# Optimization experiments

Hardware: AMD Instinct MI355X
Metric: run time of the kernel (lower is better)

## Reference

```python
import jax, jax.numpy as jnp
import numpy as np

B, S, H, NH = 4, 2048, 1024, 16
HD = H // NH

def setup_inputs() -> dict:
    key = jax.random.key(0)
    ks = jax.random.split(key, 9)
    s = 1.0 / np.sqrt(H)
    return {
        "x": jax.random.normal(ks[0], (B, S, H), dtype=jnp.float32),
        "Wq": jax.random.uniform(ks[1], (H, H), jnp.float32, -s, s),
        "bq": jax.random.uniform(ks[2], (H,), jnp.float32, -s, s),
        "Wk": jax.random.uniform(ks[3], (H, H), jnp.float32, -s, s),
        "bk": jax.random.uniform(ks[4], (H,), jnp.float32, -s, s),
        "Wv": jax.random.uniform(ks[5], (H, H), jnp.float32, -s, s),
        "bv": jax.random.uniform(ks[6], (H,), jnp.float32, -s, s),
        "Wo": jax.random.uniform(ks[7], (H, H), jnp.float32, -s, s),
        "bo": jax.random.uniform(ks[8], (H,), jnp.float32, -s, s),
    }

def reference(x, Wq, bq, Wk, bk, Wv, bv, Wo, bo):
    b, s, h = x.shape
    scale = np.sqrt(HD).astype(np.float32)
    def split_heads(t):  # [b,s,h] -> [b,nh,s,hd]
        return t.reshape(b, s, NH, HD).transpose(0, 2, 1, 3)
    Q = split_heads(x @ Wq.T + bq)
    K = split_heads(x @ Wk.T + bk)
    V = split_heads(x @ Wv.T + bv)
    scores = jnp.einsum('bnqd,bnkd->bnqk', Q, K) / scale
    weights = jax.nn.softmax(scores, axis=-1)
    attn = jnp.einsum('bnqk,bnkd->bnqd', weights, V)
    attn = attn.transpose(0, 2, 1, 3).reshape(b, s, h)
    return attn @ Wo.T + bo
```

## Files before the change

### kernel.cpp

```cpp
#include <hip/hip_runtime.h>
#include <cstdint>

#define BB 4
#define SS 2048
#define HH 1024
#define NHH 16
#define HDD 64

typedef __bf16 bf16x8 __attribute__((ext_vector_type(8)));
typedef float f32x4 __attribute__((ext_vector_type(4)));
typedef unsigned short u16x8 __attribute__((ext_vector_type(8)));

__device__ __forceinline__ unsigned short f2b(float f) {
    unsigned int u = __float_as_uint(f);
    u += 0x7fffu + ((u >> 16) & 1u);
    return (unsigned short)(u >> 16);
}

__device__ __forceinline__ void gload_lds16(const void* g, void* l) {
    __builtin_amdgcn_global_load_lds(
        (const __attribute__((address_space(1))) void*)g,
        (__attribute__((address_space(3))) void*)l, 16, 0, 0);
}

__global__ void cvt_bf16(const float* __restrict__ in,
                         unsigned short* __restrict__ out, long n) {
    long i = ((long)blockIdx.x * blockDim.x + threadIdx.x) * 4;
    long stride = (long)gridDim.x * blockDim.x * 4;
    for (; i < n; i += stride) {
        float4 v = *reinterpret_cast<const float4*>(in + i);
        ushort4 o;
        o.x = f2b(v.x); o.y = f2b(v.y); o.z = f2b(v.z); o.w = f2b(v.w);
        *reinterpret_cast<ushort4*>(out + i) = o;
    }
}

__global__ void cvt_w4(const float* __restrict__ w0, const float* __restrict__ w1,
                       const float* __restrict__ w2, const float* __restrict__ w3,
                       unsigned short* __restrict__ out) {
    const float* s = blockIdx.y == 0 ? w0 : blockIdx.y == 1 ? w1 : blockIdx.y == 2 ? w2 : w3;
    unsigned short* o = out + (size_t)blockIdx.y * ((size_t)HH * HH);
    long n = (long)HH * HH;
    long stride = (long)gridDim.x * blockDim.x * 4;
    for (long i = ((long)blockIdx.x * blockDim.x + threadIdx.x) * 4; i < n; i += stride) {
        float4 v = *reinterpret_cast<const float4*>(s + i);
        ushort4 w;
        w.x = f2b(v.x); w.y = f2b(v.y); w.z = f2b(v.z); w.w = f2b(v.w);
        *reinterpret_cast<ushort4*>(o + i) = w;
    }
}

__global__ __launch_bounds__(256) void gemm_qkv(
    const unsigned short* __restrict__ A,
    const unsigned short* __restrict__ Bqkv,
    const float* __restrict__ bq, const float* __restrict__ bk,
    const float* __restrict__ bv,
    unsigned short* __restrict__ Qo, unsigned short* __restrict__ Ko,
    unsigned short* __restrict__ Vto)
{
    __shared__ alignas(16) unsigned short Al[2][128][32];
    __shared__ alignas(16) unsigned short Bl[2][128][32];

    const int tid = threadIdx.x;
    const int lane = tid & 63;
    const int wid  = tid >> 6;
    const int wm = wid >> 1, wn = wid & 1;
    const int l15 = lane & 15, g = lane >> 4;

    const int wg = blockIdx.x;
    const int x = wg & 7;
    const int local = wg >> 3;
    const int row0 = ((x & 3) * 16 + local / 12) * 128;
    const int col0 = ((x >> 2) * 12 + local % 12) * 128;
    const int nb = col0 >> 10;
    const int cbase = col0 & 1023;
    const float* bias = nb == 0 ? bq : nb == 1 ? bk : bv;
    const int K = HH;

    f32x4 acc[4][4];
#pragma unroll
    for (int i = 0; i < 4; i++)
#pragma unroll
        for (int j = 0; j < 4; j++) acc[i][j] = (f32x4)0.0f;

    const int off0 = tid * 16;
    const int aoff0 = (off0 >> 6) * (K * 2) + (off0 & 63);
    const int off1 = off0 + 4096;
    const int aoff1 = (off1 >> 6) * (K * 2) + (off1 & 63);

    const char* gAb = (const char*)(A + (size_t)row0 * K);
    const char* gBb = (const char*)(Bqkv + (size_t)col0 * K);

    auto STAGE = [&](int buf, int k0) {
        const char* a = gAb + k0 * 64;
        const char* bsrc = gBb + k0 * 64;
        char* lA = (char*)&Al[buf][0][0] + wid * 1024;
        char* lB = (char*)&Bl[buf][0][0] + wid * 1024;
        gload_lds16(a + aoff0, lA);
        gload_lds16(a + aoff1, lA + 4096);
        gload_lds16(bsrc + aoff0, lB);
        gload_lds16(bsrc + aoff1, lB + 4096);
    };

    STAGE(0, 0);
    __syncthreads();
    int cur = 0;

    for (int k = 0; k < 32; k++) {
        if (k + 1 < 32) STAGE(cur ^ 1, k + 1);

        bf16x8 af[4], bf[4];
#pragma unroll
        for (int i = 0; i < 4; i++)
            af[i] = *reinterpret_cast<const bf16x8*>(&Al[cur][wm * 64 + i * 16 + l15][g * 8]);
#pragma unroll
        for (int j = 0; j < 4; j++)
            bf[j] = *reinterpret_cast<const bf16x8*>(&Bl[cur][wn * 64 + j * 16 + l15][g * 8]);
#pragma unroll
        for (int i = 0; i < 4; i++)
#pragma unroll
            for (int j = 0; j < 4; j++)
                acc[i][j] = __builtin_amdgcn_mfma_f32_16x16x32_bf16(af[i], bf[j], acc[i][j], 0, 0, 0);
        __syncthreads();
        cur ^= 1;
    }

#pragma unroll
    for (int i = 0; i < 4; i++) {
#pragma unroll
        for (int j = 0; j < 4; j++) {
#pragma unroll
            for (int r = 0; r < 4; r++) {
                int row = row0 + wm * 64 + i * 16 + g * 4 + r;
                int col = cbase + wn * 64 + j * 16 + l15;
                float v = acc[i][j][r] + bias[col];
                if (nb == 0) {
                    Qo[(size_t)row * HH + col] = f2b(v);
                } else if (nb == 1) {
                    Ko[(size_t)row * HH + col] = f2b(v);
                } else {
                    int b = row >> 11;
                    int s = row & (SS - 1);
                    int s6 = s & 63;
                    int sp6 = (s6 & 0x23) | ((s6 & 0x0C) << 1) | ((s6 & 0x10) >> 2);
                    int head = col >> 6;
                    int d = col & (HDD - 1);
                    size_t idx = (((size_t)b * NHH + head) * HDD + d) * SS + (s & ~63) + sp6;
                    Vto[idx] = f2b(v);
                }
            }
        }
    }
}

__global__ __launch_bounds__(256) void gemm_out(
    const unsigned short* __restrict__ A,
    const unsigned short* __restrict__ Bm,
    const float* __restrict__ bias,
    float* __restrict__ Cout,
    int M, int N, int K)
{
    __shared__ alignas(16) unsigned short Al[2][128][32];
    __shared__ alignas(16) unsigned short Bl[2][128][32];

    const int tid = threadIdx.x;
    const int lane = tid & 63;
    const int wid  = tid >> 6;
    const int wm = wid >> 1, wn = wid & 1;
    const int l15 = lane & 15, g = lane >> 4;

    const int wg = blockIdx.x;
    const int x = wg & 7;
    const int local = wg >> 3;
    const int row0 = (x * 8 + local / 8) * 128;
    const int col0 = (local % 8) * 128;

    f32x4 acc[4][4];
#pragma unroll
    for (int i = 0; i < 4; i++)
#pragma unroll
        for (int j = 0; j < 4; j++) acc[i][j] = (f32x4)0.0f;

    const int off0 = tid * 16;
    const int aoff0 = (off0 >> 6) * (K * 2) + (off0 & 63);
    const int off1 = off0 + 4096;
    const int aoff1 = (off1 >> 6) * (K * 2) + (off1 & 63);

    const char* gAb = (const char*)(A + (size_t)row0 * K);
    const char* gBb = (const char*)(Bm + (size_t)col0 * K);

    auto STAGE = [&](int buf, int k0) {
        const char* a = gAb + k0 * 64;
        const char* bsrc = gBb + k0 * 64;
        char* lA = (char*)&Al[buf][0][0] + wid * 1024;
        char* lB = (char*)&Bl[buf][0][0] + wid * 1024;
        gload_lds16(a + aoff0, lA);
        gload_lds16(a + aoff1, lA + 4096);
        gload_lds16(bsrc + aoff0, lB);
        gload_lds16(bsrc + aoff1, lB + 4096);
    };

    STAGE(0, 0);
    __syncthreads();
    int cur = 0;

    for (int k = 0; k < 32; k++) {
        if (k + 1 < 32) STAGE(cur ^ 1, k + 1);

        bf16x8 af[4], bf[4];
#pragma unroll
        for (int i = 0; i < 4; i++)
            af[i] = *reinterpret_cast<const bf16x8*>(&Al[cur][wm * 64 + i * 16 + l15][g * 8]);
#pragma unroll
        for (int j = 0; j < 4; j++)
            bf[j] = *reinterpret_cast<const bf16x8*>(&Bl[cur][wn * 64 + j * 16 + l15][g * 8]);
#pragma unroll
        for (int i = 0; i < 4; i++)
#pragma unroll
            for (int j = 0; j < 4; j++)
                acc[i][j] = __builtin_amdgcn_mfma_f32_16x16x32_bf16(af[i], bf[j], acc[i][j], 0, 0, 0);
        __syncthreads();
        cur ^= 1;
    }

#pragma unroll
    for (int i = 0; i < 4; i++) {
#pragma unroll
        for (int j = 0; j < 4; j++) {
#pragma unroll
            for (int r = 0; r < 4; r++) {
                int row = row0 + wm * 64 + i * 16 + g * 4 + r;
                int col = col0 + wn * 64 + j * 16 + l15;
                Cout[(size_t)row * N + col] = acc[i][j][r] + bias[col];
            }
        }
    }
}

__global__ __launch_bounds__(256, 4) void attn_kernel(
    const unsigned short* __restrict__ Q,
    const unsigned short* __restrict__ K,
    const unsigned short* __restrict__ Vt,
    unsigned short* __restrict__ Oa)
{
    __shared__ alignas(16) unsigned short Kf[2][8][64][8];
    __shared__ alignas(16) unsigned short Vf[2][8][64][8];

    const int tid = threadIdx.x;
    const int lane = tid & 63;
    const int wid  = tid >> 6;
    const int l15 = lane & 15, g = lane >> 4;

    const int wg = blockIdx.x;
    const int L = (wg & 7) * 128 + (wg >> 3);
    const int qt = L & 15;
    const int bh = L >> 4;
    const int b  = bh >> 4;
    const int h  = bh & 15;
    const int q0 = qt * 128;
    const int qA = q0 + wid * 32;

    const float qs = 0.125f * 1.44269504088896f;
    const unsigned short* qpA = Q + (size_t)(b * SS + qA + l15) * HH + h * HDD + g * 8;
    const unsigned short* qpB = qpA + (size_t)16 * HH;
    u16x8 ra0 = *reinterpret_cast<const u16x8*>(qpA);
    u16x8 ra1 = *reinterpret_cast<const u16x8*>(qpA + 32);
    u16x8 rb0 = *reinterpret_cast<const u16x8*>(qpB);
    u16x8 rb1 = *reinterpret_cast<const u16x8*>(qpB + 32);
#pragma unroll
    for (int j = 0; j < 8; j++) {
        ra0[j] = f2b(__uint_as_float((unsigned)ra0[j] << 16) * qs);
        ra1[j] = f2b(__uint_as_float((unsigned)ra1[j] << 16) * qs);
        rb0[j] = f2b(__uint_as_float((unsigned)rb0[j] << 16) * qs);
        rb1[j] = f2b(__uint_as_float((unsigned)rb1[j] << 16) * qs);
    }
    const bf16x8 qa0 = __builtin_bit_cast(bf16x8, ra0);
    const bf16x8 qa1 = __builtin_bit_cast(bf16x8, ra1);
    const bf16x8 qb0 = __builtin_bit_cast(bf16x8, rb0);
    const bf16x8 qb1 = __builtin_bit_cast(bf16x8, rb1);

    u16x8 ou;
#pragma unroll
    for (int j = 0; j < 8; j++) ou[j] = 0x3F80;
    const bf16x8 ones8 = __builtin_bit_cast(bf16x8, ou);
    const f32x4 zero4 = (f32x4)0.0f;

    f32x4 acc_a[4], acc_b[4];
#pragma unroll
    for (int dn = 0; dn < 4; dn++) { acc_a[dn] = zero4; acc_b[dn] = zero4; }
    float m_a = -INFINITY, m_b = -INFINITY, l_a = 0.f, l_b = 0.f;

    const int srow = tid >> 2;
    const int d0a  = (tid & 3) * 2;
    const int sfrag = ((srow >> 4) << 1) + (d0a >> 2);
    const int sslot = (srow & 15) | ((d0a & 3) << 4);

    const unsigned short* gK = K  + (size_t)(b * SS + srow) * HH + h * HDD + d0a * 8;
    const unsigned short* gV = Vt + (((size_t)b * NHH + h) * HDD + srow) * SS + d0a * 8;

    int4 kr0, kr1, vr0, vr1;

    auto stage_write = [&](int buf) {
        unsigned short* pk = &Kf[buf][sfrag][0][0] + sslot * 8;
        unsigned short* pv = &Vf[buf][sfrag][0][0] + sslot * 8;
        *reinterpret_cast<int4*>(pk)       = kr0;
        *reinterpret_cast<int4*>(pk + 128) = kr1;
        *reinterpret_cast<int4*>(pv)       = vr0;
        *reinterpret_cast<int4*>(pv + 128) = vr1;
    };

    kr0 = *reinterpret_cast<const int4*>(gK);
    kr1 = *reinterpret_cast<const int4*>(gK + 8);
    vr0 = *reinterpret_cast<const int4*>(gV);
    vr1 = *reinterpret_cast<const int4*>(gV + 8);
    stage_write(0);
    gK += (size_t)64 * HH;
    gV += 64;
    __syncthreads();

    const int NT = SS / 64;
    int cur = 0;

    for (int kt = 0; kt < NT; kt++) {
        if (kt + 1 < NT) {
            kr0 = *reinterpret_cast<const int4*>(gK);
            kr1 = *reinterpret_cast<const int4*>(gK + 8);
            vr0 = *reinterpret_cast<const int4*>(gV);
            vr1 = *reinterpret_cast<const int4*>(gV + 8);
            gK += (size_t)64 * HH;
            gV += 64;
        }

        f32x4 sa[4], sb[4];
        __builtin_amdgcn_s_setprio(1);
#pragma unroll
        for (int n = 0; n < 4; n++) {
            bf16x8 kf0 = *reinterpret_cast<const bf16x8*>(&Kf[cur][n * 2 + 0][lane][0]);
            bf16x8 kf1 = *reinterpret_cast<const bf16x8*>(&Kf[cur][n * 2 + 1][lane][0]);
            sa[n] = __builtin_amdgcn_mfma_f32_16x16x32_bf16(kf0, qa0, zero4, 0, 0, 0);
            sa[n] = __builtin_amdgcn_mfma_f32_16x16x32_bf16(kf1, qa1, sa[n], 0, 0, 0);
            sb[n] = __builtin_amdgcn_mfma_f32_16x16x32_bf16(kf0, qb0, zero4, 0, 0, 0);
            sb[n] = __builtin_amdgcn_mfma_f32_16x16x32_bf16(kf1, qb1, sb[n], 0, 0, 0);
        }
        __builtin_amdgcn_s_setprio(0);

        bf16x8 pa0, pa1, pb0, pb1;
        {
            float u0 = fmaxf(fmaxf(sa[0][0], sa[0][1]), fmaxf(sa[0][2], sa[0][3]));
            float u1 = fmaxf(fmaxf(sa[1][0], sa[1][1]), fmaxf(sa[1][2], sa[1][3]));
            float u2 = fmaxf(fmaxf(sa[2][0], sa[2][1]), fmaxf(sa[2][2], sa[2][3]));
            float u3 = fmaxf(fmaxf(sa[3][0], sa[3][1]), fmaxf(sa[3][2], sa[3][3]));
            float mt = fmaxf(fmaxf(u0, u1), fmaxf(u2, u3));
            mt = fmaxf(mt, __shfl_xor(mt, 16));
            mt = fmaxf(mt, __shfl_xor(mt, 32));
            if (!__all(mt - m_a <= 8.0f)) {
                float mnew = fmaxf(m_a, mt);
                float scl = __builtin_amdgcn_exp2f(m_a - mnew);
                m_a = mnew; l_a *= scl;
#pragma unroll
                for (int dn = 0; dn < 4; dn++)
#pragma unroll
                    for (int r = 0; r < 4; r++) acc_a[dn][r] *= scl;
            }
            float p[4][4];
#pragma unroll
            for (int n = 0; n < 4; n++)
#pragma unroll
                for (int r = 0; r < 4; r++) p[n][r] = __builtin_amdgcn_exp2f(sa[n][r] - m_a);
#pragma unroll
            for (int j = 0; j < 8; j++) {
                pa0[j] = (__bf16)p[j >> 2][j & 3];
                pa1[j] = (__bf16)p[2 + (j >> 2)][j & 3];
            }
        }
        {
            float u0 = fmaxf(fmaxf(sb[0][0], sb[0][1]), fmaxf(sb[0][2], sb[0][3]));
            float u1 = fmaxf(fmaxf(sb[1][0], sb[1][1]), fmaxf(sb[1][2], sb[1][3]));
            float u2 = fmaxf(fmaxf(sb[2][0], sb[2][1]), fmaxf(sb[2][2], sb[2][3]));
            float u3 = fmaxf(fmaxf(sb[3][0], sb[3][1]), fmaxf(sb[3][2], sb[3][3]));
            float mt = fmaxf(fmaxf(u0, u1), fmaxf(u2, u3));
            mt = fmaxf(mt, __shfl_xor(mt, 16));
            mt = fmaxf(mt, __shfl_xor(mt, 32));
            if (!__all(mt - m_b <= 8.0f)) {
                float mnew = fmaxf(m_b, mt);
                float scl = __builtin_amdgcn_exp2f(m_b - mnew);
                m_b = mnew; l_b *= scl;
#pragma unroll
                for (int dn = 0; dn < 4; dn++)
#pragma unroll
                    for (int r = 0; r < 4; r++) acc_b[dn][r] *= scl;
            }
            float p[4][4];
#pragma unroll
            for (int n = 0; n < 4; n++)
#pragma unroll
                for (int r = 0; r < 4; r++) p[n][r] = __builtin_amdgcn_exp2f(sb[n][r] - m_b);
#pragma unroll
            for (int j = 0; j < 8; j++) {
                pb0[j] = (__bf16)p[j >> 2][j & 3];
                pb1[j] = (__bf16)p[2 + (j >> 2)][j & 3];
            }
        }

        f32x4 la = zero4, lb = zero4;
        __builtin_amdgcn_s_setprio(1);
#pragma unroll
        for (int ks = 0; ks < 2; ks++) {
            bf16x8 pA = ks ? pa1 : pa0;
            bf16x8 pB = ks ? pb1 : pb0;
#pragma unroll
            for (int dn = 0; dn < 4; dn++) {
                bf16x8 vf = *reinterpret_cast<const bf16x8*>(&Vf[cur][dn * 2 + ks][lane][0]);
                acc_a[dn] = __builtin_amdgcn_mfma_f32_16x16x32_bf16(vf, pA, acc_a[dn], 0, 0, 0);
                acc_b[dn] = __builtin_amdgcn_mfma_f32_16x16x32_bf16(vf, pB, acc_b[dn], 0, 0, 0);
            }
        }
        la = __builtin_amdgcn_mfma_f32_16x16x32_bf16(ones8, pa0, la, 0, 0, 0);
        la = __builtin_amdgcn_mfma_f32_16x16x32_bf16(ones8, pa1, la, 0, 0, 0);
        lb = __builtin_amdgcn_mfma_f32_16x16x32_bf16(ones8, pb0, lb, 0, 0, 0);
        lb = __builtin_amdgcn_mfma_f32_16x16x32_bf16(ones8, pb1, lb, 0, 0, 0);
        __builtin_amdgcn_s_setprio(0);
        l_a += la[0];
        l_b += lb[0];

        if (kt + 1 < NT) stage_write(cur ^ 1);
        __syncthreads();
        cur ^= 1;
    }

    float inv_a = 1.0f / l_a;
    float inv_b = 1.0f / l_b;
    unsigned short* oA = Oa + (size_t)(b * SS + qA + l15) * HH + h * HDD;
    unsigned short* oB = oA + (size_t)16 * HH;
#pragma unroll
    for (int dn = 0; dn < 4; dn++) {
        ushort4 wa, wb;
        wa.x = f2b(acc_a[dn][0] * inv_a); wa.y = f2b(acc_a[dn][1] * inv_a);
        wa.z = f2b(acc_a[dn][2] * inv_a); wa.w = f2b(acc_a[dn][3] * inv_a);
        wb.x = f2b(acc_b[dn][0] * inv_b); wb.y = f2b(acc_b[dn][1] * inv_b);
        wb.z = f2b(acc_b[dn][2] * inv_b); wb.w = f2b(acc_b[dn][3] * inv_b);
        *reinterpret_cast<ushort4*>(oA + dn * 16 + g * 4) = wa;
        *reinterpret_cast<ushort4*>(oB + dn * 16 + g * 4) = wb;
    }
}

extern "C" void kernel_launch(void* const* d_in, const int* in_sizes, int n_in,
                              void* d_out, int out_size, void* d_ws, size_t ws_size,
                              hipStream_t stream) {
    const float* x  = (const float*)d_in[0];
    const float* Wq = (const float*)d_in[1];
    const float* bq = (const float*)d_in[2];
    const float* Wk = (const float*)d_in[3];
    const float* bk = (const float*)d_in[4];
    const float* Wv = (const float*)d_in[5];
    const float* bv = (const float*)d_in[6];
    const float* Wo = (const float*)d_in[7];
    const float* bo = (const float*)d_in[8];
    float* out = (float*)d_out;

    const int M = BB * SS;
    const long nx = (long)M * HH;

    unsigned char* ws = (unsigned char*)d_ws;
    unsigned short* xb  = (unsigned short*)(ws);
    unsigned short* Wqb = (unsigned short*)(ws + 16777216);
    unsigned short* Wob = (unsigned short*)(ws + 16777216 + 3 * 2097152);
    unsigned short* Qb  = (unsigned short*)(ws + 16777216 + 4 * 2097152);
    unsigned short* Kb  = (unsigned short*)(ws + 2 * 16777216 + 4 * 2097152);
    unsigned short* Vtb = (unsigned short*)(ws + 3 * 16777216 + 4 * 2097152);
    unsigned short* Ab  = (unsigned short*)(ws + 4 * 16777216 + 4 * 2097152);

    cvt_bf16<<<4096, 256, 0, stream>>>(x, xb, nx);
    cvt_w4<<<dim3(256, 4), 256, 0, stream>>>(Wq, Wk, Wv, Wo, Wqb);

    gemm_qkv<<<1536, 256, 0, stream>>>(xb, Wqb, bq, bk, bv, Qb, Kb, Vtb);

    attn_kernel<<<1024, 256, 0, stream>>>(Qb, Kb, Vtb, Ab);

    gemm_out<<<512, 256, 0, stream>>>(Ab, Wob, bo, out, M, HH, HH);
}
```

Before: 234.0 us.

## Use fragment-ordered LDS layout, explicit vmcnt waits, and 64x128 tiles for output GEMM

Both GEMMs now stage global tiles into LDS already laid out in MFMA fragment order, so each lane reads a contiguous 16-byte chunk instead of strided rows, which avoids bank conflicts. __syncthreads is replaced with explicit s_waitcnt vmcnt plus raw barriers, so only the previous stage's loads are waited on. The output GEMM shrinks its tile to 64x128 and launches twice as many blocks to improve occupancy and wave count. In exchange, A-tile reuse in the output GEMM drops, and the hand-written vmcnt counts must match the number of loads issued.

```diff
diff --git a/kernel.cpp b/kernel.cpp
--- a/kernel.cpp
+++ b/kernel.cpp
@@ -58,8 +58,8 @@
     unsigned short* __restrict__ Qo, unsigned short* __restrict__ Ko,
     unsigned short* __restrict__ Vto)
 {
-    __shared__ alignas(16) unsigned short Al[2][128][32];
-    __shared__ alignas(16) unsigned short Bl[2][128][32];
+    __shared__ alignas(16) unsigned short Al[2][4096];
+    __shared__ alignas(16) unsigned short Bl[2][4096];
 
     const int tid = threadIdx.x;
     const int lane = tid & 63;
@@ -76,6 +76,7 @@
     const int cbase = col0 & 1023;
     const float* bias = nb == 0 ? bq : nb == 1 ? bk : bv;
     const int K = HH;
+    const int K2 = K * 2;
 
     f32x4 acc[4][4];
 #pragma unroll
@@ -83,45 +84,54 @@
 #pragma unroll
         for (int j = 0; j < 4; j++) acc[i][j] = (f32x4)0.0f;
 
-    const int off0 = tid * 16;
-    const int aoff0 = (off0 >> 6) * (K * 2) + (off0 & 63);
-    const int off1 = off0 + 4096;
-    const int aoff1 = (off1 >> 6) * (K * 2) + (off1 & 63);
+    const int goff0 = (wid * 16 + l15) * K2 + g * 16;
+    const int goff1 = ((4 + wid) * 16 + l15) * K2 + g * 16;
 
     const char* gAb = (const char*)(A + (size_t)row0 * K);
     const char* gBb = (const char*)(Bqkv + (size_t)col0 * K);
 
-    auto STAGE = [&](int buf, int k0) {
-        const char* a = gAb + k0 * 64;
-        const char* bsrc = gBb + k0 * 64;
-        char* lA = (char*)&Al[buf][0][0] + wid * 1024;
-        char* lB = (char*)&Bl[buf][0][0] + wid * 1024;
-        gload_lds16(a + aoff0, lA);
-        gload_lds16(a + aoff1, lA + 4096);
-        gload_lds16(bsrc + aoff0, lB);
-        gload_lds16(bsrc + aoff1, lB + 4096);
+    char* Abase = (char*)&Al[0][0];
+    char* Bbase = (char*)&Bl[0][0];
+
+    auto STAGE = [&](int buf, int t) {
+        const char* a = gAb + t * 64;
+        const char* bsrc = gBb + t * 64;
+        char* lA = Abase + buf * 8192;
+        char* lB = Bbase + buf * 8192;
+        gload_lds16(a + goff0, lA + wid * 1024);
+        gload_lds16(a + goff1, lA + 4096 + wid * 1024);
+        gload_lds16(bsrc + goff0, lB + wid * 1024);
+        gload_lds16(bsrc + goff1, lB + 4096 + wid * 1024);
     };
 
     STAGE(0, 0);
-    __syncthreads();
     int cur = 0;
 
     for (int k = 0; k < 32; k++) {
-        if (k + 1 < 32) STAGE(cur ^ 1, k + 1);
-
+        if (k < 31) {
+            STAGE(cur ^ 1, k + 1);
+            asm volatile("s_waitcnt vmcnt(4)" ::: "memory");
+        } else {
+            asm volatile("s_waitcnt vmcnt(0)" ::: "memory");
+        }
+        __builtin_amdgcn_s_barrier();
+
+        const char* Ac = Abase + cur * 8192;
+        const char* Bc = Bbase + cur * 8192;
         bf16x8 af[4], bf[4];
 #pragma unroll
         for (int i = 0; i < 4; i++)
-            af[i] = *reinterpret_cast<const bf16x8*>(&Al[cur][wm * 64 + i * 16 + l15][g * 8]);
+            af[i] = *reinterpret_cast<const bf16x8*>(Ac + (wm * 4 + i) * 1024 + lane * 16);
 #pragma unroll
         for (int j = 0; j < 4; j++)
-            bf[j] = *reinterpret_cast<const bf16x8*>(&Bl[cur][wn * 64 + j * 16 + l15][g * 8]);
+            bf[j] = *reinterpret_cast<const bf16x8*>(Bc + (wn * 4 + j) * 1024 + lane * 16);
 #pragma unroll
         for (int i = 0; i < 4; i++)
 #pragma unroll
             for (int j = 0; j < 4; j++)
                 acc[i][j] = __builtin_amdgcn_mfma_f32_16x16x32_bf16(af[i], bf[j], acc[i][j], 0, 0, 0);
-        __syncthreads();
+
+        __builtin_amdgcn_s_barrier();
         cur ^= 1;
     }
 
@@ -160,77 +170,85 @@
     float* __restrict__ Cout,
     int M, int N, int K)
 {
-    __shared__ alignas(16) unsigned short Al[2][128][32];
-    __shared__ alignas(16) unsigned short Bl[2][128][32];
+    __shared__ alignas(16) unsigned short Al[2][2048];
+    __shared__ alignas(16) unsigned short Bl[2][4096];
 
     const int tid = threadIdx.x;
     const int lane = tid & 63;
     const int wid  = tid >> 6;
-    const int wm = wid >> 1, wn = wid & 1;
     const int l15 = lane & 15, g = lane >> 4;
 
     const int wg = blockIdx.x;
     const int x = wg & 7;
     const int local = wg >> 3;
-    const int row0 = (x * 8 + local / 8) * 128;
+    const int row0 = (x * 16 + local / 8) * 64;
     const int col0 = (local % 8) * 128;
-
-    f32x4 acc[4][4];
+    const int K2 = K * 2;
+
+    f32x4 acc[4][2];
 #pragma unroll
     for (int i = 0; i < 4; i++)
 #pragma unroll
-        for (int j = 0; j < 4; j++) acc[i][j] = (f32x4)0.0f;
-
-    const int off0 = tid * 16;
-    const int aoff0 = (off0 >> 6) * (K * 2) + (off0 & 63);
-    const int off1 = off0 + 4096;
-    const int aoff1 = (off1 >> 6) * (K * 2) + (off1 & 63);
+        for (int j = 0; j < 2; j++) acc[i][j] = (f32x4)0.0f;
+
+    const int goff0 = (wid * 16 + l15) * K2 + g * 16;
+    const int goff1 = ((4 + wid) * 16 + l15) * K2 + g * 16;
 
     const char* gAb = (const char*)(A + (size_t)row0 * K);
     const char* gBb = (const char*)(Bm + (size_t)col0 * K);
 
-    auto STAGE = [&](int buf, int k0) {
-        const char* a = gAb + k0 * 64;
-        const char* bsrc = gBb + k0 * 64;
-        char* lA = (char*)&Al[buf][0][0] + wid * 1024;
-        char* lB = (char*)&Bl[buf][0][0] + wid * 1024;
-        gload_lds16(a + aoff0, lA);
-        gload_lds16(a + aoff1, lA + 4096);
-        gload_lds16(bsrc + aoff0, lB);
-        gload_lds16(bsrc + aoff1, lB + 4096);
+    char* Abase = (char*)&Al[0][0];
+    char* Bbase = (char*)&Bl[0][0];
+
+    auto STAGE = [&](int buf, int t) {
+        const char* a = gAb + t * 64;
+        const char* bsrc = gBb + t * 64;
+        char* lA = Abase + buf * 4096;
+        char* lB = Bbase + buf * 8192;
+        gload_lds16(a + goff0, lA + wid * 1024);
+        gload_lds16(bsrc + goff0, lB + wid * 1024);
+        gload_lds16(bsrc + goff1, lB + 4096 + wid * 1024);
     };
 
     STAGE(0, 0);
-    __syncthreads();
     int cur = 0;
 
     for (int k = 0; k < 32; k++) {
-        if (k + 1 < 32) STAGE(cur ^ 1, k + 1);
-
-        bf16x8 af[4], bf[4];
+        if (k < 31) {
+            STAGE(cur ^ 1, k + 1);
+            asm volatile("s_waitcnt vmcnt(3)" ::: "memory");
+        } else {
+            asm volatile("s_waitcnt vmcnt(0)" ::: "memory");
+        }
+        __builtin_amdgcn_s_barrier();
+
+        const char* Ac = Abase + cur * 4096;
+        const char* Bc = Bbase + cur * 8192;
+        bf16x8 af[4], bf[2];
 #pragma unroll
         for (int i = 0; i < 4; i++)
-            af[i] = *reinterpret_cast<const bf16x8*>(&Al[cur][wm * 64 + i * 16 + l15][g * 8]);
-#pragma unroll
-        for (int j = 0; j < 4; j++)
-            bf[j] = *reinterpret_cast<const bf16x8*>(&Bl[cur][wn * 64 + j * 16 + l15][g * 8]);
+            af[i] = *reinterpret_cast<const bf16x8*>(Ac + i * 1024 + lane * 16);
+#pragma unroll
+        for (int j = 0; j < 2; j++)
+            bf[j] = *reinterpret_cast<const bf16x8*>(Bc + (wid * 2 + j) * 1024 + lane * 16);
 #pragma unroll
         for (int i = 0; i < 4; i++)
 #pragma unroll
-            for (int j = 0; j < 4; j++)
+            for (int j = 0; j < 2; j++)
                 acc[i][j] = __builtin_amdgcn_mfma_f32_16x16x32_bf16(af[i], bf[j], acc[i][j], 0, 0, 0);
-        __syncthreads();
+
+        __builtin_amdgcn_s_barrier();
         cur ^= 1;
     }
 
 #pragma unroll
     for (int i = 0; i < 4; i++) {
 #pragma unroll
-        for (int j = 0; j < 4; j++) {
+        for (int j = 0; j < 2; j++) {
 #pragma unroll
             for (int r = 0; r < 4; r++) {
-                int row = row0 + wm * 64 + i * 16 + g * 4 + r;
-                int col = col0 + wn * 64 + j * 16 + l15;
+                int row = row0 + i * 16 + g * 4 + r;
+                int col = col0 + wid * 32 + j * 16 + l15;
                 Cout[(size_t)row * N + col] = acc[i][j][r] + bias[col];
             }
         }
@@ -477,5 +495,5 @@
 
     attn_kernel<<<1024, 256, 0, stream>>>(Qb, Kb, Vtb, Ab);
 
-    gemm_out<<<512, 256, 0, stream>>>(Ab, Wob, bo, out, M, HH, HH);
-}
+    gemm_out<<<1024, 256, 0, stream>>>(Ab, Wob, bo, out, M, HH, HH);
+}
```

Measured after the change: 274.8 us. +17.5%, slower.
